# Kernel tuning notes

Hardware: AMD Instinct MI355X
Metric: run time of the kernel (lower is better)

The kernel has to match this reference:

```python
import jax, jax.numpy as jnp
import numpy as np

NH = 8          # number of attention heads
RAND_P = 0.1    # random attention probability
EPS = 1e-5      # LayerNorm eps (torch default)


def _layer_norm(x, g, b):
    m = x.mean(-1, keepdims=True)
    v = ((x - m) ** 2).mean(-1, keepdims=True)
    return (x - m) * jax.lax.rsqrt(v + EPS) * g + b


def _make_mask(u, n_frames, spatial):
    # random(0/1) + tiled-eye position mask + block-diagonal frame mask (additive float mask)
    L = n_frames * spatial
    idx = jnp.arange(L)
    frame_id = idx // spatial
    pos_id = idx % spatial
    rand = (u >= RAND_P).astype(jnp.float32)
    pos = (pos_id[:, None] == pos_id[None, :]).astype(jnp.float32)
    frame = (frame_id[:, None] == frame_id[None, :]).astype(jnp.float32)
    return rand + pos + frame  # [L, L], values in {0,1,2,3}


def _attn_block(f, u, Wqkv, bqkv, Wo, bo, g1, b1, Wfc1, bfc1, Wfc2, bfc2, g2, b2):
    N, C, H, W = f.shape
    S = H * W
    L = N * S
    hd = C // NH
    src = f.transpose(0, 2, 3, 1).reshape(L, C)  # (n,h,w) flatten order, batch=1 squeezed
    mask = _make_mask(u, N, S)

    qkv = src @ Wqkv.T + bqkv                    # [L, 3C]
    q, k, v = jnp.split(qkv, 3, axis=-1)
    q = q.reshape(L, NH, hd).transpose(1, 0, 2) * (hd ** -0.5)  # [H, L, hd]
    k = k.reshape(L, NH, hd).transpose(1, 0, 2)
    v = v.reshape(L, NH, hd).transpose(1, 0, 2)

    scores = jnp.einsum('hqd,hkd->hqk', q, k) + mask[None]      # [H, L, L]
    attn = jax.nn.softmax(scores, axis=-1)
    o = jnp.einsum('hqk,hkd->hqd', attn, v).transpose(1, 0, 2).reshape(L, C)
    src2 = o @ Wo.T + bo

    x = _layer_norm(src + src2, g1, b1)          # residual + LN (dropout p=0 -> identity)
    h = jax.nn.relu(x @ Wfc1.T + bfc1)
    x = _layer_norm(x + h @ Wfc2.T + bfc2, g2, b2)
    return x.reshape(N, H, W, C).transpose(0, 3, 1, 2)


def setup_inputs() -> dict:
    key = jax.random.key(0)
    ks = jax.random.split(key, 12)
    D = 256
    s = 0.02
    return {
        'f0': jax.random.normal(ks[0], (2, D, 80, 80), jnp.float32),
        'f1': jax.random.normal(ks[1], (2, D, 40, 40), jnp.float32),
        'f2': jax.random.normal(ks[2], (2, D, 32, 32), jnp.float32),
        'f3': jax.random.normal(ks[3], (2, D, 16, 16), jnp.float32),
        'u2': jax.random.uniform(ks[4], (2048, 2048), jnp.float32),
        'u3': jax.random.uniform(ks[5], (512, 512), jnp.float32),
        'Wqkv': jax.random.normal(ks[6], (3 * D, D), jnp.float32) * s,
        'bqkv': jnp.zeros((3 * D,), jnp.float32),
        'Wo': jax.random.normal(ks[7], (D, D), jnp.float32) * s,
        'bo': jnp.zeros((D,), jnp.float32),
        'g1': jnp.ones((D,), jnp.float32),
        'b1': jnp.zeros((D,), jnp.float32),
        'Wfc1': jax.random.normal(ks[8], (4 * D, D), jnp.float32) * s,
        'bfc1': jnp.zeros((4 * D,), jnp.float32),
        'Wfc2': jax.random.normal(ks[9], (D, 4 * D), jnp.float32) * s,
        'bfc2': jnp.zeros((D,), jnp.float32),
        'g2': jnp.ones((D,), jnp.float32),
        'b2': jnp.zeros((D,), jnp.float32),
    }


def reference(f0, f1, f2, f3, u2, u3, Wqkv, bqkv, Wo, bo, g1, b1,
              Wfc1, bfc1, Wfc2, bfc2, g2, b2):
    params = (Wqkv, bqkv, Wo, bo, g1, b1, Wfc1, bfc1, Wfc2, bfc2, g2, b2)
    # levels 0 and 1 pass through untouched (loop starts at i=2)
    out2 = _attn_block(f2, u2, *params)
    out3 = _attn_block(f3, u3, *params)
    return (f0, f1, out2, out3)
```

## Files before the change

kernel.cpp:

```cpp
#include <hip/hip_runtime.h>
#include <hip/hip_bf16.h>
#include <cstddef>


typedef __attribute__((ext_vector_type(8))) short s16x8;
typedef __attribute__((ext_vector_type(4))) short s16x4;
typedef __attribute__((ext_vector_type(4))) float f32x4;
typedef __attribute__((ext_vector_type(2))) unsigned int u32x2;
typedef unsigned short ushort_t;
typedef unsigned long long u64;

#define RTOT 2560

__device__ inline unsigned short f2bf(float x) {
    union { __hip_bfloat16 h; unsigned short u; } cv;
    cv.h = __float2bfloat16(x);
    return cv.u;
}
__device__ inline float bf2f(unsigned short u) {
    union { unsigned int i; float f; } cv;
    cv.i = ((unsigned int)u) << 16;
    return cv.f;
}

__global__ __launch_bounds__(256) void prep(const float* __restrict__ wqkv,
                                            const float* __restrict__ wo,
                                            const float* __restrict__ wfc1,
                                            const float* __restrict__ wfc2,
                                            ushort_t* __restrict__ o1,
                                            ushort_t* __restrict__ o2,
                                            ushort_t* __restrict__ o3,
                                            ushort_t* __restrict__ o4,
                                            const float* __restrict__ u2,
                                            const float* __restrict__ u3,
                                            u64* __restrict__ ub,
                                            const float* __restrict__ f2,
                                            const float* __restrict__ f3,
                                            float* __restrict__ srcf,
                                            ushort_t* __restrict__ srcb) {
    int bid = blockIdx.x;
    int t = threadIdx.x;
    if (bid < 768) {
        int i = bid * 256 + t;
        const float* src; ushort_t* dst; int li;
        if (i < 49152)       { src = wqkv; dst = o1; li = i; }
        else if (i < 65536)  { src = wo;   dst = o2; li = i - 49152; }
        else if (i < 131072) { src = wfc1; dst = o3; li = i - 65536; }
        else                 { src = wfc2; dst = o4; li = i - 131072; }
        f32x4 v = ((const f32x4*)src)[li];
        s16x4 r;
        r[0] = (short)f2bf(v[0]); r[1] = (short)f2bf(v[1]);
        r[2] = (short)f2bf(v[2]); r[3] = (short)f2bf(v[3]);
        ((s16x4*)dst)[li] = r;
    } else if (bid < 18176) {
        int gw = ((bid - 768) * 256 + t) >> 6;
        int lane = t & 63;
        float v;
        if (gw < 65536) v = u2[(size_t)gw * 64 + lane];
        else            v = u3[(size_t)(gw - 65536) * 64 + lane];
        u64 b = __ballot(v >= 0.1f);
        if (lane == 0) ub[gw] = b;
    } else {
        int idx = (bid - 18176) * 256 + t;
        int r = idx >> 8, c = idx & 255;
        float v;
        if (r < 2048) {
            int n = r >> 10, hw = r & 1023;
            v = f2[(size_t)((n * 256 + c) << 10) + hw];
        } else {
            int rl = r - 2048;
            int n = rl >> 8, hw = rl & 255;
            v = f3[(size_t)((n * 256 + c) << 8) + hw];
        }
        srcf[idx] = v;
        srcb[idx] = f2bf(v);
    }
}

__global__ __launch_bounds__(256) void lc_out(const float* __restrict__ y,
                                              float* __restrict__ out2,
                                              float* __restrict__ out3) {
    int idx = blockIdx.x * 256 + threadIdx.x;
    if (idx < 524288) {
        int n = idx >> 18;
        int rem = idx & 262143;
        int c = rem >> 10, hw = rem & 1023;
        out2[idx] = y[(size_t)(n * 1024 + hw) * 256 + c];
    } else {
        int li = idx - 524288;
        int n = li >> 16;
        int rem = li & 65535;
        int c = rem >> 8, hw = rem & 255;
        out3[li] = y[(size_t)(2048 + n * 256 + hw) * 256 + c];
    }
}

#define ASTR 72

template <int EPI, int OUTBF>
__global__ __launch_bounds__(128) void gemm32(const ushort_t* __restrict__ A,
                                              const ushort_t* __restrict__ W,
                                              const float* __restrict__ bias,
                                              const float* __restrict__ res,
                                              void* __restrict__ outv,
                                              int M, int N, int K) {
    __shared__ __align__(16) ushort_t As[2][32 * ASTR];
    __shared__ __align__(16) ushort_t Ws[2][32 * ASTR];

    const int t = threadIdx.x;
    const int w = t >> 6, l = t & 63;
    const int c = l & 15, g = l >> 4;
    const int m0 = blockIdx.y * 32, n0 = blockIdx.x * 32;
    const int srow = t >> 3;
    const int cg8 = (t & 7) * 8;

    const ushort_t* Aip0 = &A[(size_t)(m0 + srow) * K + cg8];
    const ushort_t* Aip1 = &A[(size_t)(m0 + 16 + srow) * K + cg8];
    const ushort_t* Wip0 = &W[(size_t)(n0 + srow) * K + cg8];
    const ushort_t* Wip1 = &W[(size_t)(n0 + 16 + srow) * K + cg8];

    s16x8 ra0 = *(const s16x8*)Aip0;
    s16x8 ra1 = *(const s16x8*)Aip1;
    s16x8 rw0 = *(const s16x8*)Wip0;
    s16x8 rw1 = *(const s16x8*)Wip1;
    *(s16x8*)&As[0][srow * ASTR + cg8] = ra0;
    *(s16x8*)&As[0][(16 + srow) * ASTR + cg8] = ra1;
    *(s16x8*)&Ws[0][srow * ASTR + cg8] = rw0;
    *(s16x8*)&Ws[0][(16 + srow) * ASTR + cg8] = rw1;
    __syncthreads();

    f32x4 acc[2] = {{0.f, 0.f, 0.f, 0.f}, {0.f, 0.f, 0.f, 0.f}};
    const int nsteps = K >> 6;

    for (int ks = 0; ks < nsteps; ++ks) {
        const int b = ks & 1;
        const bool pf = (ks + 1 < nsteps);
        if (pf) {
            int ko = (ks + 1) << 6;
            ra0 = *(const s16x8*)(Aip0 + ko);
            ra1 = *(const s16x8*)(Aip1 + ko);
            rw0 = *(const s16x8*)(Wip0 + ko);
            rw1 = *(const s16x8*)(Wip1 + ko);
        }
#pragma unroll
        for (int kt = 0; kt < 2; ++kt) {
            s16x8 af = *(const s16x8*)&As[b][(16 * w + c) * ASTR + kt * 32 + 8 * g];
            s16x8 wf0 = *(const s16x8*)&Ws[b][c * ASTR + kt * 32 + 8 * g];
            s16x8 wf1 = *(const s16x8*)&Ws[b][(16 + c) * ASTR + kt * 32 + 8 * g];
            acc[0] = __builtin_amdgcn_mfma_f32_16x16x32_bf16(af, wf0, acc[0], 0, 0, 0);
            acc[1] = __builtin_amdgcn_mfma_f32_16x16x32_bf16(af, wf1, acc[1], 0, 0, 0);
        }
        if (pf) {
            int nb = b ^ 1;
            *(s16x8*)&As[nb][srow * ASTR + cg8] = ra0;
            *(s16x8*)&As[nb][(16 + srow) * ASTR + cg8] = ra1;
            *(s16x8*)&Ws[nb][srow * ASTR + cg8] = rw0;
            *(s16x8*)&Ws[nb][(16 + srow) * ASTR + cg8] = rw1;
        }
        __syncthreads();
    }

#pragma unroll
    for (int nt = 0; nt < 2; ++nt) {
        int n = n0 + 16 * nt + c;
        float bv = bias[n];
        float sc = 1.f;
        if (EPI == 3) sc = (n < 256) ? 0.17677669529663687f : 1.f;
#pragma unroll
        for (int r = 0; r < 4; ++r) {
            int m = m0 + 16 * w + 4 * g + r;
            float v = acc[nt][r] + bv;
            if (EPI == 1) v = fmaxf(v, 0.f);
            if (EPI == 2) v += res[(size_t)m * N + n];
            if (EPI == 3) v *= sc;
            if (OUTBF) ((ushort_t*)outv)[(size_t)m * N + n] = f2bf(v);
            else ((float*)outv)[(size_t)m * N + n] = v;
        }
    }
}

template <int EPI, int OUTBF>
__global__ __launch_bounds__(256) void gemm64(const ushort_t* __restrict__ A,
                                              const ushort_t* __restrict__ W,
                                              const float* __restrict__ bias,
                                              const float* __restrict__ res,
                                              void* __restrict__ outv,
                                              int M, int N, int K) {
    __shared__ __align__(16) ushort_t As[2][64 * ASTR];
    __shared__ __align__(16) ushort_t Ws[2][64 * ASTR];

    const int t = threadIdx.x;
    const int w = t >> 6, l = t & 63;
    const int c = l & 15, g = l >> 4;
    const int mh = w >> 1, nh = w & 1;
    const int m0 = blockIdx.y * 64, n0 = blockIdx.x * 64;
    const int srow = t >> 3;
    const int cg8 = (t & 7) * 8;

    const ushort_t* Aip0 = &A[(size_t)(m0 + srow) * K + cg8];
    const ushort_t* Aip1 = &A[(size_t)(m0 + 32 + srow) * K + cg8];
    const ushort_t* Wip0 = &W[(size_t)(n0 + srow) * K + cg8];
    const ushort_t* Wip1 = &W[(size_t)(n0 + 32 + srow) * K + cg8];

    s16x8 ra0 = *(const s16x8*)Aip0;
    s16x8 ra1 = *(const s16x8*)Aip1;
    s16x8 rw0 = *(const s16x8*)Wip0;
    s16x8 rw1 = *(const s16x8*)Wip1;
    *(s16x8*)&As[0][srow * ASTR + cg8] = ra0;
    *(s16x8*)&As[0][(32 + srow) * ASTR + cg8] = ra1;
    *(s16x8*)&Ws[0][srow * ASTR + cg8] = rw0;
    *(s16x8*)&Ws[0][(32 + srow) * ASTR + cg8] = rw1;
    __syncthreads();

    f32x4 acc[2][2] = {{{0.f,0.f,0.f,0.f},{0.f,0.f,0.f,0.f}},
                       {{0.f,0.f,0.f,0.f},{0.f,0.f,0.f,0.f}}};
    const int nsteps = K >> 6;

    for (int ks = 0; ks < nsteps; ++ks) {
        const int b = ks & 1;
        const bool pf = (ks + 1 < nsteps);
        if (pf) {
            int ko = (ks + 1) << 6;
            ra0 = *(const s16x8*)(Aip0 + ko);
            ra1 = *(const s16x8*)(Aip1 + ko);
            rw0 = *(const s16x8*)(Wip0 + ko);
            rw1 = *(const s16x8*)(Wip1 + ko);
        }
#pragma unroll
        for (int sl = 0; sl < 2; ++sl) {
            s16x8 af0 = *(const s16x8*)&As[b][(32 * mh + c) * ASTR + sl * 32 + 8 * g];
            s16x8 af1 = *(const s16x8*)&As[b][(32 * mh + 16 + c) * ASTR + sl * 32 + 8 * g];
            s16x8 wf0 = *(const s16x8*)&Ws[b][(32 * nh + c) * ASTR + sl * 32 + 8 * g];
            s16x8 wf1 = *(const s16x8*)&Ws[b][(32 * nh + 16 + c) * ASTR + sl * 32 + 8 * g];
            acc[0][0] = __builtin_amdgcn_mfma_f32_16x16x32_bf16(af0, wf0, acc[0][0], 0, 0, 0);
            acc[0][1] = __builtin_amdgcn_mfma_f32_16x16x32_bf16(af0, wf1, acc[0][1], 0, 0, 0);
            acc[1][0] = __builtin_amdgcn_mfma_f32_16x16x32_bf16(af1, wf0, acc[1][0], 0, 0, 0);
            acc[1][1] = __builtin_amdgcn_mfma_f32_16x16x32_bf16(af1, wf1, acc[1][1], 0, 0, 0);
        }
        if (pf) {
            int nb = b ^ 1;
            *(s16x8*)&As[nb][srow * ASTR + cg8] = ra0;
            *(s16x8*)&As[nb][(32 + srow) * ASTR + cg8] = ra1;
            *(s16x8*)&Ws[nb][srow * ASTR + cg8] = rw0;
            *(s16x8*)&Ws[nb][(32 + srow) * ASTR + cg8] = rw1;
        }
        __syncthreads();
    }

#pragma unroll
    for (int i = 0; i < 2; ++i)
#pragma unroll
    for (int j = 0; j < 2; ++j) {
        int n = n0 + 32 * nh + 16 * j + c;
        float bv = bias[n];
        float sc = 1.f;
        if (EPI == 3) sc = (n < 256) ? 0.17677669529663687f : 1.f;
#pragma unroll
        for (int r = 0; r < 4; ++r) {
            int m = m0 + 32 * mh + 16 * i + 4 * g + r;
            float v = acc[i][j][r] + bv;
            if (EPI == 1) v = fmaxf(v, 0.f);
            if (EPI == 2) v += res[(size_t)m * N + n];
            if (EPI == 3) v *= sc;
            if (OUTBF) ((ushort_t*)outv)[(size_t)m * N + n] = f2bf(v);
            else ((float*)outv)[(size_t)m * N + n] = v;
        }
    }
}

#define QS 40
#define KS 40
#define VS 66
#define PS 72
#define OS 68

__global__ __launch_bounds__(256) void flash_split(const ushort_t* __restrict__ qkvb,
                                                   const u64* __restrict__ ubits,
                                                   ushort_t* __restrict__ Opart,
                                                   float2* __restrict__ ml) {
    __shared__ __align__(16) ushort_t qs[64 * QS];
    __shared__ __align__(16) ushort_t ks[2][64 * KS];
    __shared__ __align__(16) ushort_t vts[2][32 * VS];
    __shared__ __align__(16) char pso[64 * PS * 2];
    ushort_t* ps = (ushort_t*)pso;
    float* os = (float*)pso;

    const int bx = blockIdx.x;
    int qt, h, split, L, sshift, rowbase, wpr;
    const u64* ub;
    if (bx < 1024) {
        qt = bx & 31; h = (bx >> 5) & 7; split = bx >> 8;
        L = 2048; sshift = 10; rowbase = 0; wpr = 32; ub = ubits;
    } else {
        int lo = bx - 1024;
        qt = lo & 7; h = (lo >> 3) & 7; split = lo >> 6;
        L = 512; sshift = 8; rowbase = 2048; wpr = 8; ub = ubits + 65536;
    }
    const int tps = (L >> 6) >> 2;
    const int ts0 = split * tps;

    const int t = threadIdx.x;
    const int w = t >> 6;
    const int l = t & 63;
    const int c = l & 15;
    const int g = l >> 4;
    const int smask = (1 << sshift) - 1;

    const int srow = t >> 2;
    const int sc8 = (t & 3) * 8;
    const int q0g = rowbase + qt * 64;

    *(s16x8*)&qs[srow * QS + sc8] =
        *(const s16x8*)&qkvb[(size_t)(q0g + srow) * 768 + h * 32 + sc8];

    {
        size_t base = (size_t)(rowbase + ts0 * 64 + srow) * 768 + h * 32 + sc8;
        s16x8 kreg = *(const s16x8*)&qkvb[base + 256];
        s16x8 vreg = *(const s16x8*)&qkvb[base + 512];
        *(s16x8*)&ks[0][srow * KS + sc8] = kreg;
#pragma unroll
        for (int i = 0; i < 8; ++i)
            vts[0][(sc8 + i) * VS + srow] = (ushort_t)vreg[i];
    }
    __syncthreads();

    const s16x8 qf = *(const s16x8*)&qs[(16 * w + c) * QS + 8 * g];
    const int ql = qt * 64 + 16 * w + c;
    const int qp = ql & smask, qfr = ql >> sshift;
    const u64* ubq = &ub[(size_t)ql * wpr];

    f32x4 oacc0 = {0.f, 0.f, 0.f, 0.f};
    f32x4 oacc1 = {0.f, 0.f, 0.f, 0.f};
    float mold = -3e38f, lrun = 0.f;
    const f32x4 zc = {0.f, 0.f, 0.f, 0.f};

    for (int kt = 0; kt < tps; ++kt) {
        const int bb = kt & 1;
        const int k0 = (ts0 + kt) << 6;
        const bool pf = (kt + 1 < tps);

        u64 wq = ubq[ts0 + kt];

        s16x8 kreg, vreg;
        if (pf) {
            size_t base = (size_t)(rowbase + k0 + 64 + srow) * 768 + h * 32 + sc8;
            kreg = *(const s16x8*)&qkvb[base + 256];
            vreg = *(const s16x8*)&qkvb[base + 512];
        }

        f32x4 sacc[4];
#pragma unroll
        for (int nt = 0; nt < 4; ++nt) {
            s16x8 kf = *(const s16x8*)&ks[bb][(16 * nt + c) * KS + 8 * g];
            sacc[nt] = __builtin_amdgcn_mfma_f32_16x16x32_bf16(kf, qf, zc, 0, 0, 0);
        }

        float sv[4][4];
        float m = -3e38f;
#pragma unroll
        for (int nt = 0; nt < 4; ++nt) {
            unsigned nib = (unsigned)(wq >> (16 * nt + 4 * g));
#pragma unroll
            for (int r = 0; r < 4; ++r) {
                int kg = k0 + 16 * nt + 4 * g + r;
                float s = sacc[nt][r]
                        + ((nib >> r) & 1 ? 1.f : 0.f)
                        + ((kg & smask) == qp ? 1.f : 0.f)
                        + ((kg >> sshift) == qfr ? 1.f : 0.f);
                sv[nt][r] = s;
                m = fmaxf(m, s);
            }
        }
        m = fmaxf(m, __shfl_xor(m, 16));
        m = fmaxf(m, __shfl_xor(m, 32));
        float newm = fmaxf(mold, m);
        float fac = __expf(mold - newm);
        mold = newm;

        float sum = 0.f;
#pragma unroll
        for (int nt = 0; nt < 4; ++nt) {
            float p0 = __expf(sv[nt][0] - newm);
            float p1 = __expf(sv[nt][1] - newm);
            float p2 = __expf(sv[nt][2] - newm);
            float p3 = __expf(sv[nt][3] - newm);
            sum += (p0 + p1) + (p2 + p3);
            u32x2 pk;
            pk[0] = ((unsigned)f2bf(p1) << 16) | f2bf(p0);
            pk[1] = ((unsigned)f2bf(p3) << 16) | f2bf(p2);
            *(u32x2*)&ps[(16 * w + c) * PS + 16 * nt + 4 * g] = pk;
        }
        sum += __shfl_xor(sum, 16);
        sum += __shfl_xor(sum, 32);
        lrun = lrun * fac + sum;
        oacc0 *= fac;
        oacc1 *= fac;

#pragma unroll
        for (int kc = 0; kc < 2; ++kc) {
            s16x8 pfr = *(const s16x8*)&ps[(16 * w + c) * PS + 32 * kc + 8 * g];
            s16x8 vf0 = *(const s16x8*)&vts[bb][c * VS + 32 * kc + 8 * g];
            s16x8 vf1 = *(const s16x8*)&vts[bb][(16 + c) * VS + 32 * kc + 8 * g];
            oacc0 = __builtin_amdgcn_mfma_f32_16x16x32_bf16(vf0, pfr, oacc0, 0, 0, 0);
            oacc1 = __builtin_amdgcn_mfma_f32_16x16x32_bf16(vf1, pfr, oacc1, 0, 0, 0);
        }

        __syncthreads();
        if (pf) {
            int nb = bb ^ 1;
            *(s16x8*)&ks[nb][srow * KS + sc8] = kreg;
#pragma unroll
            for (int i = 0; i < 8; ++i)
                vts[nb][(sc8 + i) * VS + srow] = (ushort_t)vreg[i];
        }
        __syncthreads();
    }

    if (g == 0) {
        int q = q0g + 16 * w + c;
        ml[((size_t)split * RTOT + q) * 8 + h] = make_float2(mold, lrun);
    }

#pragma unroll
    for (int r = 0; r < 4; ++r) {
        os[(4 * g + r) * OS + 16 * w + c] = oacc0[r];
        os[(16 + 4 * g + r) * OS + 16 * w + c] = oacc1[r];
    }
    __syncthreads();
    {
        int r = t >> 2, d0 = (t & 3) * 8;
        s16x8 pk;
#pragma unroll
        for (int i = 0; i < 8; ++i) pk[i] = (short)f2bf(os[(d0 + i) * OS + r]);
        *(s16x8*)&Opart[((size_t)split * RTOT + q0g + r) * 256 + h * 32 + d0] = pk;
    }
}

__global__ __launch_bounds__(256) void flash_merge(const ushort_t* __restrict__ Opart,
                                                   const float2* __restrict__ ml,
                                                   ushort_t* __restrict__ obuf) {
    int r = blockIdx.x, t = threadIdx.x;
    int h = t >> 5;
    float2 m0 = ml[((size_t)0 * RTOT + r) * 8 + h];
    float2 m1 = ml[((size_t)1 * RTOT + r) * 8 + h];
    float2 m2 = ml[((size_t)2 * RTOT + r) * 8 + h];
    float2 m3 = ml[((size_t)3 * RTOT + r) * 8 + h];
    float ms = fmaxf(fmaxf(m0.x, m1.x), fmaxf(m2.x, m3.x));
    float w0 = __expf(m0.x - ms), w1 = __expf(m1.x - ms);
    float w2 = __expf(m2.x - ms), w3 = __expf(m3.x - ms);
    float denom = w0 * m0.y + w1 * m1.y + w2 * m2.y + w3 * m3.y;
    size_t idx = (size_t)r * 256 + t;
    const size_t stride = (size_t)RTOT * 256;
    float v = w0 * bf2f(Opart[idx]) + w1 * bf2f(Opart[idx + stride])
            + w2 * bf2f(Opart[idx + 2 * stride]) + w3 * bf2f(Opart[idx + 3 * stride]);
    obuf[idx] = f2bf(v / denom);
}

template <int WB>
__global__ __launch_bounds__(256) void ln_kernel(const float* __restrict__ in,
                                                 const float* __restrict__ g,
                                                 const float* __restrict__ b,
                                                 float* __restrict__ outf,
                                                 ushort_t* __restrict__ outb) {
    __shared__ float red[256];
    int row = blockIdx.x, t = threadIdx.x;
    float v = in[(size_t)row * 256 + t];
    red[t] = v;
    __syncthreads();
    for (int s = 128; s > 0; s >>= 1) {
        if (t < s) red[t] += red[t + s];
        __syncthreads();
    }
    float mean = red[0] * (1.f / 256.f);
    __syncthreads();
    float d = v - mean;
    red[t] = d * d;
    __syncthreads();
    for (int s = 128; s > 0; s >>= 1) {
        if (t < s) red[t] += red[t + s];
        __syncthreads();
    }
    float var = red[0] * (1.f / 256.f);
    float r = d * rsqrtf(var + 1e-5f) * g[t] + b[t];
    outf[(size_t)row * 256 + t] = r;
    if (WB) outb[(size_t)row * 256 + t] = f2bf(r);
}


extern "C" void kernel_launch(void* const* d_in, const int* in_sizes, int n_in,
                              void* d_out, int out_size, void* d_ws, size_t ws_size,
                              hipStream_t stream) {
    const float* f0 = (const float*)d_in[0];
    const float* f1 = (const float*)d_in[1];
    const float* f2 = (const float*)d_in[2];
    const float* f3 = (const float*)d_in[3];
    const float* u2 = (const float*)d_in[4];
    const float* u3 = (const float*)d_in[5];
    const float* Wqkv = (const float*)d_in[6];
    const float* bqkv = (const float*)d_in[7];
    const float* Wo   = (const float*)d_in[8];
    const float* bo   = (const float*)d_in[9];
    const float* g1   = (const float*)d_in[10];
    const float* b1   = (const float*)d_in[11];
    const float* Wfc1 = (const float*)d_in[12];
    const float* bfc1 = (const float*)d_in[13];
    const float* Wfc2 = (const float*)d_in[14];
    const float* bfc2 = (const float*)d_in[15];
    const float* g2   = (const float*)d_in[16];
    const float* b2   = (const float*)d_in[17];

    float* out = (float*)d_out;
    float* ws = (float*)d_ws;

    ushort_t* wqkv = (ushort_t*)ws;
    ushort_t* wo   = (ushort_t*)(ws + 98304);
    ushort_t* wfc1 = (ushort_t*)(ws + 131072);
    ushort_t* wfc2 = (ushort_t*)(ws + 262144);

    float* sc = ws + 393216;
    float*    src_f32 = sc;
    ushort_t* qkvb    = (ushort_t*)(sc + 655360);
    ushort_t* obuf    = (ushort_t*)(sc + 1638400);
    ushort_t* src_bf  = obuf;
    float*    t1      = sc + 1966080;
    float*    x_f32   = sc + 2621440;
    u64*      ubits   = (u64*)x_f32;
    ushort_t* x_bf    = (ushort_t*)(sc + 3276800);
    float2*   ml      = (float2*)(sc + 3604480);
    ushort_t* Opart   = (ushort_t*)(sc + 3768320);
    ushort_t* h_bf    = Opart;
    float*    y       = src_f32;

    prep<<<20736, 256, 0, stream>>>(Wqkv, Wo, Wfc1, Wfc2, wqkv, wo, wfc1, wfc2,
                                    u2, u3, ubits, f2, f3, src_f32, src_bf);

    hipMemcpyAsync(out, f0, (size_t)3276800 * 4, hipMemcpyDeviceToDevice, stream);
    hipMemcpyAsync(out + 3276800, f1, (size_t)819200 * 4, hipMemcpyDeviceToDevice, stream);

    gemm64<3, 1><<<dim3(12, 40), 256, 0, stream>>>(
        src_bf, wqkv, bqkv, nullptr, qkvb, RTOT, 768, 256);
    flash_split<<<1280, 256, 0, stream>>>(qkvb, ubits, Opart, ml);
    flash_merge<<<2560, 256, 0, stream>>>(Opart, ml, obuf);
    gemm32<2, 0><<<dim3(8, 80), 128, 0, stream>>>(
        obuf, wo, bo, src_f32, t1, RTOT, 256, 256);
    ln_kernel<1><<<2560, 256, 0, stream>>>(t1, g1, b1, x_f32, x_bf);
    gemm64<1, 1><<<dim3(16, 40), 256, 0, stream>>>(
        x_bf, wfc1, bfc1, nullptr, h_bf, RTOT, 1024, 256);
    gemm32<2, 0><<<dim3(8, 80), 128, 0, stream>>>(
        h_bf, wfc2, bfc2, x_f32, t1, RTOT, 256, 1024);
    ln_kernel<0><<<2560, 256, 0, stream>>>(t1, g2, b2, y, nullptr);
    lc_out<<<2560, 256, 0, stream>>>(y, out + 4096000, out + 4620288);
}
```

Measured before the change: 96.73 us.

## Fuse passthrough copies, flash merge, and output transpose into neighboring kernels

Moves the f0/f1 passthrough copies out of two memcpy calls and into the prep kernel. Vectorizes the random-mask bit packing, now four ballots per wave with a new bit layout consumed by flash_split. Folds the split-softmax merge into the A-operand load of the Wo GEMM and fuses the final layout transpose into the second LayerNorm, which removes two launches and their intermediate buffers. The flash kernel's K/V double-buffering is also reordered to use a single barrier per tile. In exchange, the Wo GEMM recomputes the merge weights for every tile column, repeating exp work and Opart reads across its eight column blocks.

```diff
diff --git a/kernel.cpp b/kernel.cpp
--- a/kernel.cpp
+++ b/kernel.cpp
@@ -23,7 +23,10 @@
     return cv.f;
 }
 
-__global__ __launch_bounds__(256) void prep(const float* __restrict__ wqkv,
+__global__ __launch_bounds__(256) void prep(const float* __restrict__ f0,
+                                            const float* __restrict__ f1,
+                                            float* __restrict__ outp,
+                                            const float* __restrict__ wqkv,
                                             const float* __restrict__ wo,
                                             const float* __restrict__ wfc1,
                                             const float* __restrict__ wfc2,
@@ -40,8 +43,13 @@
                                             ushort_t* __restrict__ srcb) {
     int bid = blockIdx.x;
     int t = threadIdx.x;
-    if (bid < 768) {
-        int i = bid * 256 + t;
+    if (bid < 4000) {
+        int idx = bid * 256 + t;
+        f32x4 v = (idx < 819200) ? ((const f32x4*)f0)[idx]
+                                 : ((const f32x4*)f1)[idx - 819200];
+        ((f32x4*)outp)[idx] = v;
+    } else if (bid < 4768) {
+        int i = (bid - 4000) * 256 + t;
         const float* src; ushort_t* dst; int li;
         if (i < 49152)       { src = wqkv; dst = o1; li = i; }
         else if (i < 65536)  { src = wo;   dst = o2; li = i - 49152; }
@@ -52,16 +60,32 @@
         r[0] = (short)f2bf(v[0]); r[1] = (short)f2bf(v[1]);
         r[2] = (short)f2bf(v[2]); r[3] = (short)f2bf(v[3]);
         ((s16x4*)dst)[li] = r;
-    } else if (bid < 18176) {
-        int gw = ((bid - 768) * 256 + t) >> 6;
+    } else if (bid < 9120) {
+        int gw = ((bid - 4768) * 256 + t) >> 6;
         int lane = t & 63;
-        float v;
-        if (gw < 65536) v = u2[(size_t)gw * 64 + lane];
-        else            v = u3[(size_t)(gw - 65536) * 64 + lane];
-        u64 b = __ballot(v >= 0.1f);
-        if (lane == 0) ub[gw] = b;
+        const float* p;
+        u64* dst;
+        if (gw < 16384) {
+            int row = gw >> 3, ch = gw & 7;
+            p = &u2[(size_t)row * 2048 + ch * 256 + lane * 4];
+            dst = &ub[(size_t)gw * 4];
+        } else {
+            int lw = gw - 16384;
+            int row = lw >> 1, ch = lw & 1;
+            p = &u3[(size_t)row * 512 + ch * 256 + lane * 4];
+            dst = &ub[65536 + (size_t)lw * 4];
+        }
+        f32x4 v = *(const f32x4*)p;
+        u64 b0 = __ballot(v[0] >= 0.1f);
+        u64 b1 = __ballot(v[1] >= 0.1f);
+        u64 b2 = __ballot(v[2] >= 0.1f);
+        u64 b3 = __ballot(v[3] >= 0.1f);
+        if (lane < 4) {
+            u64 bb = (lane == 0) ? b0 : (lane == 1) ? b1 : (lane == 2) ? b2 : b3;
+            dst[lane] = bb;
+        }
     } else {
-        int idx = (bid - 18176) * 256 + t;
+        int idx = (bid - 9120) * 256 + t;
         int r = idx >> 8, c = idx & 255;
         float v;
         if (r < 2048) {
@@ -77,59 +101,42 @@
     }
 }
 
-__global__ __launch_bounds__(256) void lc_out(const float* __restrict__ y,
-                                              float* __restrict__ out2,
-                                              float* __restrict__ out3) {
-    int idx = blockIdx.x * 256 + threadIdx.x;
-    if (idx < 524288) {
-        int n = idx >> 18;
-        int rem = idx & 262143;
-        int c = rem >> 10, hw = rem & 1023;
-        out2[idx] = y[(size_t)(n * 1024 + hw) * 256 + c];
-    } else {
-        int li = idx - 524288;
-        int n = li >> 16;
-        int rem = li & 65535;
-        int c = rem >> 8, hw = rem & 255;
-        out3[li] = y[(size_t)(2048 + n * 256 + hw) * 256 + c];
-    }
-}
-
 #define ASTR 72
 
-template <int EPI, int OUTBF>
-__global__ __launch_bounds__(128) void gemm32(const ushort_t* __restrict__ A,
+template <int EPI>
+__global__ __launch_bounds__(256) void gemm64(const ushort_t* __restrict__ A,
                                               const ushort_t* __restrict__ W,
                                               const float* __restrict__ bias,
-                                              const float* __restrict__ res,
-                                              void* __restrict__ outv,
+                                              ushort_t* __restrict__ outb,
                                               int M, int N, int K) {
-    __shared__ __align__(16) ushort_t As[2][32 * ASTR];
-    __shared__ __align__(16) ushort_t Ws[2][32 * ASTR];
+    __shared__ __align__(16) ushort_t As[2][64 * ASTR];
+    __shared__ __align__(16) ushort_t Ws[2][64 * ASTR];
 
     const int t = threadIdx.x;
     const int w = t >> 6, l = t & 63;
     const int c = l & 15, g = l >> 4;
-    const int m0 = blockIdx.y * 32, n0 = blockIdx.x * 32;
+    const int mh = w >> 1, nh = w & 1;
+    const int m0 = blockIdx.y * 64, n0 = blockIdx.x * 64;
     const int srow = t >> 3;
     const int cg8 = (t & 7) * 8;
 
     const ushort_t* Aip0 = &A[(size_t)(m0 + srow) * K + cg8];
-    const ushort_t* Aip1 = &A[(size_t)(m0 + 16 + srow) * K + cg8];
+    const ushort_t* Aip1 = &A[(size_t)(m0 + 32 + srow) * K + cg8];
     const ushort_t* Wip0 = &W[(size_t)(n0 + srow) * K + cg8];
-    const ushort_t* Wip1 = &W[(size_t)(n0 + 16 + srow) * K + cg8];
+    const ushort_t* Wip1 = &W[(size_t)(n0 + 32 + srow) * K + cg8];
 
     s16x8 ra0 = *(const s16x8*)Aip0;
     s16x8 ra1 = *(const s16x8*)Aip1;
     s16x8 rw0 = *(const s16x8*)Wip0;
     s16x8 rw1 = *(const s16x8*)Wip1;
     *(s16x8*)&As[0][srow * ASTR + cg8] = ra0;
-    *(s16x8*)&As[0][(16 + srow) * ASTR + cg8] = ra1;
+    *(s16x8*)&As[0][(32 + srow) * ASTR + cg8] = ra1;
     *(s16x8*)&Ws[0][srow * ASTR + cg8] = rw0;
-    *(s16x8*)&Ws[0][(16 + srow) * ASTR + cg8] = rw1;
-    __syncthreads();
-
-    f32x4 acc[2] = {{0.f, 0.f, 0.f, 0.f}, {0.f, 0.f, 0.f, 0.f}};
+    *(s16x8*)&Ws[0][(32 + srow) * ASTR + cg8] = rw1;
+    __syncthreads();
+
+    f32x4 acc[2][2] = {{{0.f,0.f,0.f,0.f},{0.f,0.f,0.f,0.f}},
+                       {{0.f,0.f,0.f,0.f},{0.f,0.f,0.f,0.f}}};
     const int nsteps = K >> 6;
 
     for (int ks = 0; ks < nsteps; ++ks) {
@@ -143,77 +150,77 @@
             rw1 = *(const s16x8*)(Wip1 + ko);
         }
 #pragma unroll
-        for (int kt = 0; kt < 2; ++kt) {
-            s16x8 af = *(const s16x8*)&As[b][(16 * w + c) * ASTR + kt * 32 + 8 * g];
-            s16x8 wf0 = *(const s16x8*)&Ws[b][c * ASTR + kt * 32 + 8 * g];
-            s16x8 wf1 = *(const s16x8*)&Ws[b][(16 + c) * ASTR + kt * 32 + 8 * g];
-            acc[0] = __builtin_amdgcn_mfma_f32_16x16x32_bf16(af, wf0, acc[0], 0, 0, 0);
-            acc[1] = __builtin_amdgcn_mfma_f32_16x16x32_bf16(af, wf1, acc[1], 0, 0, 0);
+        for (int sl = 0; sl < 2; ++sl) {
+            s16x8 af0 = *(const s16x8*)&As[b][(32 * mh + c) * ASTR + sl * 32 + 8 * g];
+            s16x8 af1 = *(const s16x8*)&As[b][(32 * mh + 16 + c) * ASTR + sl * 32 + 8 * g];
+            s16x8 wf0 = *(const s16x8*)&Ws[b][(32 * nh + c) * ASTR + sl * 32 + 8 * g];
+            s16x8 wf1 = *(const s16x8*)&Ws[b][(32 * nh + 16 + c) * ASTR + sl * 32 + 8 * g];
+            acc[0][0] = __builtin_amdgcn_mfma_f32_16x16x32_bf16(af0, wf0, acc[0][0], 0, 0, 0);
+            acc[0][1] = __builtin_amdgcn_mfma_f32_16x16x32_bf16(af0, wf1, acc[0][1], 0, 0, 0);
+            acc[1][0] = __builtin_amdgcn_mfma_f32_16x16x32_bf16(af1, wf0, acc[1][0], 0, 0, 0);
+            acc[1][1] = __builtin_amdgcn_mfma_f32_16x16x32_bf16(af1, wf1, acc[1][1], 0, 0, 0);
         }
         if (pf) {
             int nb = b ^ 1;
             *(s16x8*)&As[nb][srow * ASTR + cg8] = ra0;
-            *(s16x8*)&As[nb][(16 + srow) * ASTR + cg8] = ra1;
+            *(s16x8*)&As[nb][(32 + srow) * ASTR + cg8] = ra1;
             *(s16x8*)&Ws[nb][srow * ASTR + cg8] = rw0;
-            *(s16x8*)&Ws[nb][(16 + srow) * ASTR + cg8] = rw1;
-        }
-        __syncthreads();
-    }
-
-#pragma unroll
-    for (int nt = 0; nt < 2; ++nt) {
-        int n = n0 + 16 * nt + c;
+            *(s16x8*)&Ws[nb][(32 + srow) * ASTR + cg8] = rw1;
+        }
+        __syncthreads();
+    }
+
+#pragma unroll
+    for (int i = 0; i < 2; ++i)
+#pragma unroll
+    for (int j = 0; j < 2; ++j) {
+        int n = n0 + 32 * nh + 16 * j + c;
         float bv = bias[n];
         float sc = 1.f;
         if (EPI == 3) sc = (n < 256) ? 0.17677669529663687f : 1.f;
 #pragma unroll
         for (int r = 0; r < 4; ++r) {
-            int m = m0 + 16 * w + 4 * g + r;
-            float v = acc[nt][r] + bv;
+            int m = m0 + 32 * mh + 16 * i + 4 * g + r;
+            float v = acc[i][j][r] + bv;
             if (EPI == 1) v = fmaxf(v, 0.f);
-            if (EPI == 2) v += res[(size_t)m * N + n];
             if (EPI == 3) v *= sc;
-            if (OUTBF) ((ushort_t*)outv)[(size_t)m * N + n] = f2bf(v);
-            else ((float*)outv)[(size_t)m * N + n] = v;
-        }
-    }
-}
-
-template <int EPI, int OUTBF>
-__global__ __launch_bounds__(256) void gemm64(const ushort_t* __restrict__ A,
-                                              const ushort_t* __restrict__ W,
-                                              const float* __restrict__ bias,
-                                              const float* __restrict__ res,
-                                              void* __restrict__ outv,
-                                              int M, int N, int K) {
-    __shared__ __align__(16) ushort_t As[2][64 * ASTR];
-    __shared__ __align__(16) ushort_t Ws[2][64 * ASTR];
+            outb[(size_t)m * N + n] = f2bf(v);
+        }
+    }
+}
+
+__global__ __launch_bounds__(128) void gemm_fc2(const ushort_t* __restrict__ A,
+                                                const ushort_t* __restrict__ W,
+                                                const float* __restrict__ bias,
+                                                const float* __restrict__ res,
+                                                float* __restrict__ outf,
+                                                int M, int N, int K) {
+    __shared__ __align__(16) ushort_t As[2][32 * ASTR];
+    __shared__ __align__(16) ushort_t Ws[2][32 * ASTR];
 
     const int t = threadIdx.x;
     const int w = t >> 6, l = t & 63;
     const int c = l & 15, g = l >> 4;
-    const int mh = w >> 1, nh = w & 1;
-    const int m0 = blockIdx.y * 64, n0 = blockIdx.x * 64;
+    const int m0 = blockIdx.y * 32, n0 = blockIdx.x * 32;
     const int srow = t >> 3;
     const int cg8 = (t & 7) * 8;
 
     const ushort_t* Aip0 = &A[(size_t)(m0 + srow) * K + cg8];
-    const ushort_t* Aip1 = &A[(size_t)(m0 + 32 + srow) * K + cg8];
+    const ushort_t* Aip1 = &A[(size_t)(m0 + 16 + srow) * K + cg8];
     const ushort_t* Wip0 = &W[(size_t)(n0 + srow) * K + cg8];
-    const ushort_t* Wip1 = &W[(size_t)(n0 + 32 + srow) * K + cg8];
+    const ushort_t* Wip1 = &W[(size_t)(n0 + 16 + srow) * K + cg8];
 
     s16x8 ra0 = *(const s16x8*)Aip0;
     s16x8 ra1 = *(const s16x8*)Aip1;
     s16x8 rw0 = *(const s16x8*)Wip0;
     s16x8 rw1 = *(const s16x8*)Wip1;
     *(s16x8*)&As[0][srow * ASTR + cg8] = ra0;
-    *(s16x8*)&As[0][(32 + srow) * ASTR + cg8] = ra1;
+    *(s16x8*)&As[0][(16 + srow) * ASTR + cg8] = ra1;
     *(s16x8*)&Ws[0][srow * ASTR + cg8] = rw0;
-    *(s16x8*)&Ws[0][(32 + srow) * ASTR + cg8] = rw1;
-    __syncthreads();
-
-    f32x4 acc[2][2] = {{{0.f,0.f,0.f,0.f},{0.f,0.f,0.f,0.f}},
-                       {{0.f,0.f,0.f,0.f},{0.f,0.f,0.f,0.f}}};
+    *(s16x8*)&Ws[0][(16 + srow) * ASTR + cg8] = rw1;
+    __syncthreads();
+
+    f32x4 acc[2] = {{0.f, 0.f, 0.f, 0.f}, {0.f, 0.f, 0.f, 0.f}};
     const int nsteps = K >> 6;
 
     for (int ks = 0; ks < nsteps; ++ks) {
@@ -227,43 +234,131 @@
             rw1 = *(const s16x8*)(Wip1 + ko);
         }
 #pragma unroll
-        for (int sl = 0; sl < 2; ++sl) {
-            s16x8 af0 = *(const s16x8*)&As[b][(32 * mh + c) * ASTR + sl * 32 + 8 * g];
-            s16x8 af1 = *(const s16x8*)&As[b][(32 * mh + 16 + c) * ASTR + sl * 32 + 8 * g];
-            s16x8 wf0 = *(const s16x8*)&Ws[b][(32 * nh + c) * ASTR + sl * 32 + 8 * g];
-            s16x8 wf1 = *(const s16x8*)&Ws[b][(32 * nh + 16 + c) * ASTR + sl * 32 + 8 * g];
-            acc[0][0] = __builtin_amdgcn_mfma_f32_16x16x32_bf16(af0, wf0, acc[0][0], 0, 0, 0);
-            acc[0][1] = __builtin_amdgcn_mfma_f32_16x16x32_bf16(af0, wf1, acc[0][1], 0, 0, 0);
-            acc[1][0] = __builtin_amdgcn_mfma_f32_16x16x32_bf16(af1, wf0, acc[1][0], 0, 0, 0);
-            acc[1][1] = __builtin_amdgcn_mfma_f32_16x16x32_bf16(af1, wf1, acc[1][1], 0, 0, 0);
+        for (int kt = 0; kt < 2; ++kt) {
+            s16x8 af = *(const s16x8*)&As[b][(16 * w + c) * ASTR + kt * 32 + 8 * g];
+            s16x8 wf0 = *(const s16x8*)&Ws[b][c * ASTR + kt * 32 + 8 * g];
+            s16x8 wf1 = *(const s16x8*)&Ws[b][(16 + c) * ASTR + kt * 32 + 8 * g];
+            acc[0] = __builtin_amdgcn_mfma_f32_16x16x32_bf16(af, wf0, acc[0], 0, 0, 0);
+            acc[1] = __builtin_amdgcn_mfma_f32_16x16x32_bf16(af, wf1, acc[1], 0, 0, 0);
         }
         if (pf) {
             int nb = b ^ 1;
             *(s16x8*)&As[nb][srow * ASTR + cg8] = ra0;
-            *(s16x8*)&As[nb][(32 + srow) * ASTR + cg8] = ra1;
+            *(s16x8*)&As[nb][(16 + srow) * ASTR + cg8] = ra1;
             *(s16x8*)&Ws[nb][srow * ASTR + cg8] = rw0;
-            *(s16x8*)&Ws[nb][(32 + srow) * ASTR + cg8] = rw1;
-        }
-        __syncthreads();
-    }
-
-#pragma unroll
-    for (int i = 0; i < 2; ++i)
-#pragma unroll
-    for (int j = 0; j < 2; ++j) {
-        int n = n0 + 32 * nh + 16 * j + c;
+            *(s16x8*)&Ws[nb][(16 + srow) * ASTR + cg8] = rw1;
+        }
+        __syncthreads();
+    }
+
+#pragma unroll
+    for (int nt = 0; nt < 2; ++nt) {
+        int n = n0 + 16 * nt + c;
         float bv = bias[n];
-        float sc = 1.f;
-        if (EPI == 3) sc = (n < 256) ? 0.17677669529663687f : 1.f;
 #pragma unroll
         for (int r = 0; r < 4; ++r) {
-            int m = m0 + 32 * mh + 16 * i + 4 * g + r;
-            float v = acc[i][j][r] + bv;
-            if (EPI == 1) v = fmaxf(v, 0.f);
-            if (EPI == 2) v += res[(size_t)m * N + n];
-            if (EPI == 3) v *= sc;
-            if (OUTBF) ((ushort_t*)outv)[(size_t)m * N + n] = f2bf(v);
-            else ((float*)outv)[(size_t)m * N + n] = v;
+            int m = m0 + 16 * w + 4 * g + r;
+            float v = acc[nt][r] + bv + res[(size_t)m * N + n];
+            outf[(size_t)m * N + n] = v;
+        }
+    }
+}
+
+__global__ __launch_bounds__(128) void gemm_wo(const ushort_t* __restrict__ Opart,
+                                               const float2* __restrict__ ml,
+                                               const ushort_t* __restrict__ W,
+                                               const float* __restrict__ bias,
+                                               const float* __restrict__ res,
+                                               float* __restrict__ outf) {
+    const int K = 256, N = 256;
+    __shared__ __align__(16) ushort_t As[2][32 * ASTR];
+    __shared__ __align__(16) ushort_t Ws[2][32 * ASTR];
+
+    const int t = threadIdx.x;
+    const int w = t >> 6, l = t & 63;
+    const int c = l & 15, g = l >> 4;
+    const int m0 = blockIdx.y * 32, n0 = blockIdx.x * 32;
+    const int srow = t >> 3;
+    const int cg8 = (t & 7) * 8;
+
+    auto loadA = [&](int row, int kcol) -> s16x8 {
+        int head = kcol >> 5;
+        float2 a0 = ml[((size_t)0 * RTOT + row) * 8 + head];
+        float2 a1 = ml[((size_t)1 * RTOT + row) * 8 + head];
+        float2 a2 = ml[((size_t)2 * RTOT + row) * 8 + head];
+        float2 a3 = ml[((size_t)3 * RTOT + row) * 8 + head];
+        float M = fmaxf(fmaxf(a0.x, a1.x), fmaxf(a2.x, a3.x));
+        float w1 = __expf(a0.x - M), w2 = __expf(a1.x - M);
+        float w3 = __expf(a2.x - M), w4 = __expf(a3.x - M);
+        float inv = 1.f / (w1 * a0.y + w2 * a1.y + w3 * a2.y + w4 * a3.y);
+        const size_t str = (size_t)RTOT * 256;
+        size_t base = (size_t)row * 256 + kcol;
+        s16x8 o1 = *(const s16x8*)&Opart[base];
+        s16x8 o2 = *(const s16x8*)&Opart[base + str];
+        s16x8 o3 = *(const s16x8*)&Opart[base + 2 * str];
+        s16x8 o4 = *(const s16x8*)&Opart[base + 3 * str];
+        s16x8 r;
+#pragma unroll
+        for (int e = 0; e < 8; ++e) {
+            float v = w1 * bf2f((ushort_t)o1[e]) + w2 * bf2f((ushort_t)o2[e])
+                    + w3 * bf2f((ushort_t)o3[e]) + w4 * bf2f((ushort_t)o4[e]);
+            r[e] = (short)f2bf(v * inv);
+        }
+        return r;
+    };
+
+    const ushort_t* Wip0 = &W[(size_t)(n0 + srow) * K + cg8];
+    const ushort_t* Wip1 = &W[(size_t)(n0 + 16 + srow) * K + cg8];
+
+    s16x8 ra0 = loadA(m0 + srow, cg8);
+    s16x8 ra1 = loadA(m0 + 16 + srow, cg8);
+    s16x8 rw0 = *(const s16x8*)Wip0;
+    s16x8 rw1 = *(const s16x8*)Wip1;
+    *(s16x8*)&As[0][srow * ASTR + cg8] = ra0;
+    *(s16x8*)&As[0][(16 + srow) * ASTR + cg8] = ra1;
+    *(s16x8*)&Ws[0][srow * ASTR + cg8] = rw0;
+    *(s16x8*)&Ws[0][(16 + srow) * ASTR + cg8] = rw1;
+    __syncthreads();
+
+    f32x4 acc[2] = {{0.f, 0.f, 0.f, 0.f}, {0.f, 0.f, 0.f, 0.f}};
+    const int nsteps = 4;
+
+    for (int ks = 0; ks < nsteps; ++ks) {
+        const int b = ks & 1;
+        const bool pf = (ks + 1 < nsteps);
+        if (pf) {
+            int ko = (ks + 1) << 6;
+            ra0 = loadA(m0 + srow, ko + cg8);
+            ra1 = loadA(m0 + 16 + srow, ko + cg8);
+            rw0 = *(const s16x8*)(Wip0 + ko);
+            rw1 = *(const s16x8*)(Wip1 + ko);
+        }
+#pragma unroll
+        for (int kt = 0; kt < 2; ++kt) {
+            s16x8 af = *(const s16x8*)&As[b][(16 * w + c) * ASTR + kt * 32 + 8 * g];
+            s16x8 wf0 = *(const s16x8*)&Ws[b][c * ASTR + kt * 32 + 8 * g];
+            s16x8 wf1 = *(const s16x8*)&Ws[b][(16 + c) * ASTR + kt * 32 + 8 * g];
+            acc[0] = __builtin_amdgcn_mfma_f32_16x16x32_bf16(af, wf0, acc[0], 0, 0, 0);
+            acc[1] = __builtin_amdgcn_mfma_f32_16x16x32_bf16(af, wf1, acc[1], 0, 0, 0);
+        }
+        if (pf) {
+            int nb = b ^ 1;
+            *(s16x8*)&As[nb][srow * ASTR + cg8] = ra0;
+            *(s16x8*)&As[nb][(16 + srow) * ASTR + cg8] = ra1;
+            *(s16x8*)&Ws[nb][srow * ASTR + cg8] = rw0;
+            *(s16x8*)&Ws[nb][(16 + srow) * ASTR + cg8] = rw1;
+        }
+        __syncthreads();
+    }
+
+#pragma unroll
+    for (int nt = 0; nt < 2; ++nt) {
+        int n = n0 + 16 * nt + c;
+        float bv = bias[n];
+#pragma unroll
+        for (int r = 0; r < 4; ++r) {
+            int m = m0 + 16 * w + 4 * g + r;
+            outf[(size_t)m * 256 + n] = acc[nt][r] + bv + res[(size_t)m * 256 + n];
         }
     }
 }
@@ -279,25 +374,26 @@
                                                    ushort_t* __restrict__ Opart,
                                                    float2* __restrict__ ml) {
     __shared__ __align__(16) ushort_t qs[64 * QS];
-    __shared__ __align__(16) ushort_t ks[2][64 * KS];
-    __shared__ __align__(16) ushort_t vts[2][32 * VS];
+    __shared__ __align__(16) ushort_t ks[3][64 * KS];
+    __shared__ __align__(16) ushort_t vts[3][32 * VS];
     __shared__ __align__(16) char pso[64 * PS * 2];
     ushort_t* ps = (ushort_t*)pso;
     float* os = (float*)pso;
 
     const int bx = blockIdx.x;
-    int qt, h, split, L, sshift, rowbase, wpr;
+    int qt, h, split, L, sshift, rowbase;
     const u64* ub;
     if (bx < 1024) {
         qt = bx & 31; h = (bx >> 5) & 7; split = bx >> 8;
-        L = 2048; sshift = 10; rowbase = 0; wpr = 32; ub = ubits;
+        L = 2048; sshift = 10; rowbase = 0; ub = ubits;
     } else {
         int lo = bx - 1024;
         qt = lo & 7; h = (lo >> 3) & 7; split = lo >> 6;
-        L = 512; sshift = 8; rowbase = 2048; wpr = 8; ub = ubits + 65536;
+        L = 512; sshift = 8; rowbase = 2048; ub = ubits + 65536;
     }
     const int tps = (L >> 6) >> 2;
     const int ts0 = split * tps;
+    const int nch = L >> 8;
 
     const int t = threadIdx.x;
     const int w = t >> 6;
@@ -313,45 +409,61 @@
     *(s16x8*)&qs[srow * QS + sc8] =
         *(const s16x8*)&qkvb[(size_t)(q0g + srow) * 768 + h * 32 + sc8];
 
+    s16x8 kreg, vreg;
     {
         size_t base = (size_t)(rowbase + ts0 * 64 + srow) * 768 + h * 32 + sc8;
-        s16x8 kreg = *(const s16x8*)&qkvb[base + 256];
-        s16x8 vreg = *(const s16x8*)&qkvb[base + 512];
-        *(s16x8*)&ks[0][srow * KS + sc8] = kreg;
+        s16x8 k0r = *(const s16x8*)&qkvb[base + 256];
+        s16x8 v0r = *(const s16x8*)&qkvb[base + 512];
+        *(s16x8*)&ks[0][srow * KS + sc8] = k0r;
 #pragma unroll
         for (int i = 0; i < 8; ++i)
-            vts[0][(sc8 + i) * VS + srow] = (ushort_t)vreg[i];
+            vts[0][(sc8 + i) * VS + srow] = (ushort_t)v0r[i];
+        if (tps > 1) {
+            kreg = *(const s16x8*)&qkvb[base + 64 * 768 + 256];
+            vreg = *(const s16x8*)&qkvb[base + 64 * 768 + 512];
+        }
     }
     __syncthreads();
 
     const s16x8 qf = *(const s16x8*)&qs[(16 * w + c) * QS + 8 * g];
     const int ql = qt * 64 + 16 * w + c;
     const int qp = ql & smask, qfr = ql >> sshift;
-    const u64* ubq = &ub[(size_t)ql * wpr];
+    const u64* ubq = &ub[(size_t)ql * nch * 4];
 
     f32x4 oacc0 = {0.f, 0.f, 0.f, 0.f};
     f32x4 oacc1 = {0.f, 0.f, 0.f, 0.f};
     float mold = -3e38f, lrun = 0.f;
     const f32x4 zc = {0.f, 0.f, 0.f, 0.f};
 
+    u64 wr0 = 0, wr1 = 0, wr2 = 0, wr3 = 0;
+    int cur = 0;
     for (int kt = 0; kt < tps; ++kt) {
-        const int bb = kt & 1;
-        const int k0 = (ts0 + kt) << 6;
-        const bool pf = (kt + 1 < tps);
-
-        u64 wq = ubq[ts0 + kt];
-
-        s16x8 kreg, vreg;
-        if (pf) {
-            size_t base = (size_t)(rowbase + k0 + 64 + srow) * 768 + h * 32 + sc8;
+        int nxt = cur + 1; if (nxt == 3) nxt = 0;
+        const int gt = ts0 + kt;
+        const int k0 = gt << 6;
+
+        if (kt + 1 < tps) {
+            *(s16x8*)&ks[nxt][srow * KS + sc8] = kreg;
+#pragma unroll
+            for (int i = 0; i < 8; ++i)
+                vts[nxt][(sc8 + i) * VS + srow] = (ushort_t)vreg[i];
+        }
+        if (kt + 2 < tps) {
+            size_t base = (size_t)(rowbase + (gt + 2) * 64 + srow) * 768 + h * 32 + sc8;
             kreg = *(const s16x8*)&qkvb[base + 256];
             vreg = *(const s16x8*)&qkvb[base + 512];
         }
 
+        if ((gt & 3) == 0 || kt == 0) {
+            const u64* bp = &ubq[(size_t)(gt >> 2) * 4];
+            wr0 = bp[0]; wr1 = bp[1]; wr2 = bp[2]; wr3 = bp[3];
+        }
+        const unsigned shb = 16 * (gt & 3);
+
         f32x4 sacc[4];
 #pragma unroll
         for (int nt = 0; nt < 4; ++nt) {
-            s16x8 kf = *(const s16x8*)&ks[bb][(16 * nt + c) * KS + 8 * g];
+            s16x8 kf = *(const s16x8*)&ks[cur][(16 * nt + c) * KS + 8 * g];
             sacc[nt] = __builtin_amdgcn_mfma_f32_16x16x32_bf16(kf, qf, zc, 0, 0, 0);
         }
 
@@ -359,12 +471,13 @@
         float m = -3e38f;
 #pragma unroll
         for (int nt = 0; nt < 4; ++nt) {
-            unsigned nib = (unsigned)(wq >> (16 * nt + 4 * g));
+            unsigned sh = shb + 4 * nt + g;
 #pragma unroll
             for (int r = 0; r < 4; ++r) {
+                u64 wrd = (r == 0) ? wr0 : (r == 1) ? wr1 : (r == 2) ? wr2 : wr3;
                 int kg = k0 + 16 * nt + 4 * g + r;
                 float s = sacc[nt][r]
-                        + ((nib >> r) & 1 ? 1.f : 0.f)
+                        + ((wrd >> sh) & 1 ? 1.f : 0.f)
                         + ((kg & smask) == qp ? 1.f : 0.f)
                         + ((kg >> sshift) == qfr ? 1.f : 0.f);
                 sv[nt][r] = s;
@@ -399,21 +512,14 @@
 #pragma unroll
         for (int kc = 0; kc < 2; ++kc) {
             s16x8 pfr = *(const s16x8*)&ps[(16 * w + c) * PS + 32 * kc + 8 * g];
-            s16x8 vf0 = *(const s16x8*)&vts[bb][c * VS + 32 * kc + 8 * g];
-            s16x8 vf1 = *(const s16x8*)&vts[bb][(16 + c) * VS + 32 * kc + 8 * g];
+            s16x8 vf0 = *(const s16x8*)&vts[cur][c * VS + 32 * kc + 8 * g];
+            s16x8 vf1 = *(const s16x8*)&vts[cur][(16 + c) * VS + 32 * kc + 8 * g];
             oacc0 = __builtin_amdgcn_mfma_f32_16x16x32_bf16(vf0, pfr, oacc0, 0, 0, 0);
             oacc1 = __builtin_amdgcn_mfma_f32_16x16x32_bf16(vf1, pfr, oacc1, 0, 0, 0);
         }
 
         __syncthreads();
-        if (pf) {
-            int nb = bb ^ 1;
-            *(s16x8*)&ks[nb][srow * KS + sc8] = kreg;
-#pragma unroll
-            for (int i = 0; i < 8; ++i)
-                vts[nb][(sc8 + i) * VS + srow] = (ushort_t)vreg[i];
-        }
-        __syncthreads();
+        cur = nxt;
     }
 
     if (g == 0) {
@@ -436,32 +542,11 @@
     }
 }
 
-__global__ __launch_bounds__(256) void flash_merge(const ushort_t* __restrict__ Opart,
-                                                   const float2* __restrict__ ml,
-                                                   ushort_t* __restrict__ obuf) {
-    int r = blockIdx.x, t = threadIdx.x;
-    int h = t >> 5;
-    float2 m0 = ml[((size_t)0 * RTOT + r) * 8 + h];
-    float2 m1 = ml[((size_t)1 * RTOT + r) * 8 + h];
-    float2 m2 = ml[((size_t)2 * RTOT + r) * 8 + h];
-    float2 m3 = ml[((size_t)3 * RTOT + r) * 8 + h];
-    float ms = fmaxf(fmaxf(m0.x, m1.x), fmaxf(m2.x, m3.x));
-    float w0 = __expf(m0.x - ms), w1 = __expf(m1.x - ms);
-    float w2 = __expf(m2.x - ms), w3 = __expf(m3.x - ms);
-    float denom = w0 * m0.y + w1 * m1.y + w2 * m2.y + w3 * m3.y;
-    size_t idx = (size_t)r * 256 + t;
-    const size_t stride = (size_t)RTOT * 256;
-    float v = w0 * bf2f(Opart[idx]) + w1 * bf2f(Opart[idx + stride])
-            + w2 * bf2f(Opart[idx + 2 * stride]) + w3 * bf2f(Opart[idx + 3 * stride]);
-    obuf[idx] = f2bf(v / denom);
-}
-
-template <int WB>
-__global__ __launch_bounds__(256) void ln_kernel(const float* __restrict__ in,
-                                                 const float* __restrict__ g,
-                                                 const float* __restrict__ b,
-                                                 float* __restrict__ outf,
-                                                 ushort_t* __restrict__ outb) {
+__global__ __launch_bounds__(256) void ln1_kernel(const float* __restrict__ in,
+                                                  const float* __restrict__ g,
+                                                  const float* __restrict__ b,
+                                                  float* __restrict__ outf,
+                                                  ushort_t* __restrict__ outb) {
     __shared__ float red[256];
     int row = blockIdx.x, t = threadIdx.x;
     float v = in[(size_t)row * 256 + t];
@@ -483,7 +568,42 @@
     float var = red[0] * (1.f / 256.f);
     float r = d * rsqrtf(var + 1e-5f) * g[t] + b[t];
     outf[(size_t)row * 256 + t] = r;
-    if (WB) outb[(size_t)row * 256 + t] = f2bf(r);
+    outb[(size_t)row * 256 + t] = f2bf(r);
+}
+
+__global__ __launch_bounds__(256) void ln2_out(const float* __restrict__ in,
+                                               const float* __restrict__ g,
+                                               const float* __restrict__ b,
+                                               float* __restrict__ out2,
+                                               float* __restrict__ out3) {
+    __shared__ float red[256];
+    int row = blockIdx.x, t = threadIdx.x;
+    float v = in[(size_t)row * 256 + t];
+    red[t] = v;
+    __syncthreads();
+    for (int s = 128; s > 0; s >>= 1) {
+        if (t < s) red[t] += red[t + s];
+        __syncthreads();
+    }
+    float mean = red[0] * (1.f / 256.f);
+    __syncthreads();
+    float d = v - mean;
+    red[t] = d * d;
+    __syncthreads();
+    for (int s = 128; s > 0; s >>= 1) {
+        if (t < s) red[t] += red[t + s];
+        __syncthreads();
+    }
+    float var = red[0] * (1.f / 256.f);
+    float r = d * rsqrtf(var + 1e-5f) * g[t] + b[t];
+    if (row < 2048) {
+        int n = row >> 10, hw = row & 1023;
+        out2[((size_t)(n * 256 + t) << 10) + hw] = r;
+    } else {
+        int rl = row - 2048;
+        int n = rl >> 8, hw = rl & 255;
+        out3[((size_t)(n * 256 + t) << 8) + hw] = r;
+    }
 }
 
 
@@ -520,8 +640,7 @@
     float* sc = ws + 393216;
     float*    src_f32 = sc;
     ushort_t* qkvb    = (ushort_t*)(sc + 655360);
-    ushort_t* obuf    = (ushort_t*)(sc + 1638400);
-    ushort_t* src_bf  = obuf;
+    ushort_t* src_bf  = (ushort_t*)(sc + 1638400);
     float*    t1      = sc + 1966080;
     float*    x_f32   = sc + 2621440;
     u64*      ubits   = (u64*)x_f32;
@@ -529,25 +648,19 @@
     float2*   ml      = (float2*)(sc + 3604480);
     ushort_t* Opart   = (ushort_t*)(sc + 3768320);
     ushort_t* h_bf    = Opart;
-    float*    y       = src_f32;
-
-    prep<<<20736, 256, 0, stream>>>(Wqkv, Wo, Wfc1, Wfc2, wqkv, wo, wfc1, wfc2,
+
+    prep<<<11680, 256, 0, stream>>>(f0, f1, out,
+                                    Wqkv, Wo, Wfc1, Wfc2, wqkv, wo, wfc1, wfc2,
                                     u2, u3, ubits, f2, f3, src_f32, src_bf);
 
-    hipMemcpyAsync(out, f0, (size_t)3276800 * 4, hipMemcpyDeviceToDevice, stream);
-    hipMemcpyAsync(out + 3276800, f1, (size_t)819200 * 4, hipMemcpyDeviceToDevice, stream);
-
-    gemm64<3, 1><<<dim3(12, 40), 256, 0, stream>>>(
-        src_bf, wqkv, bqkv, nullptr, qkvb, RTOT, 768, 256);
+    gemm64<3><<<dim3(12, 40), 256, 0, stream>>>(
+        src_bf, wqkv, bqkv, qkvb, RTOT, 768, 256);
     flash_split<<<1280, 256, 0, stream>>>(qkvb, ubits, Opart, ml);
-    flash_merge<<<2560, 256, 0, stream>>>(Opart, ml, obuf);
-    gemm32<2, 0><<<dim3(8, 80), 128, 0, stream>>>(
-        obuf, wo, bo, src_f32, t1, RTOT, 256, 256);
-    ln_kernel<1><<<2560, 256, 0, stream>>>(t1, g1, b1, x_f32, x_bf);
-    gemm64<1, 1><<<dim3(16, 40), 256, 0, stream>>>(
-        x_bf, wfc1, bfc1, nullptr, h_bf, RTOT, 1024, 256);
-    gemm32<2, 0><<<dim3(8, 80), 128, 0, stream>>>(
+    gemm_wo<<<dim3(8, 80), 128, 0, stream>>>(Opart, ml, wo, bo, src_f32, t1);
+    ln1_kernel<<<2560, 256, 0, stream>>>(t1, g1, b1, x_f32, x_bf);
+    gemm64<1><<<dim3(16, 40), 256, 0, stream>>>(
+        x_bf, wfc1, bfc1, h_bf, RTOT, 1024, 256);
+    gemm_fc2<<<dim3(8, 80), 128, 0, stream>>>(
         h_bf, wfc2, bfc2, x_f32, t1, RTOT, 256, 1024);
-    ln_kernel<0><<<2560, 256, 0, stream>>>(t1, g2, b2, y, nullptr);
-    lc_out<<<2560, 256, 0, stream>>>(y, out + 4096000, out + 4620288);
-}
+    ln2_out<<<2560, 256, 0, stream>>>(t1, g2, b2, out + 4096000, out + 4620288);
+}
```

Result: no change. 96.40 us (-0.3%).
